# Kernel optimization log

Hardware: AMD Instinct MI355X
Metric: run time of the kernel (lower is better)

The kernel has to match this reference:

```python
import jax, jax.numpy as jnp
import numpy as np

B, T, D, H, L, V = 2, 1024, 768, 12, 8, 32000
HD = D // H


def setup_inputs() -> dict:
    key = jax.random.key(0)
    ks = jax.random.split(key, 16)
    init = lambda k, shape: jax.random.normal(k, shape, jnp.float32) * 0.02
    return {
        "idx": jax.random.randint(ks[0], (B, T), 0, V),
        "targets": jax.random.randint(ks[1], (B, T), 0, V),
        "tok_emb": init(ks[2], (V, D)),
        "pos_emb": init(ks[3], (T, D)),
        "ln1_w": jnp.ones((L, D)), "ln1_b": jnp.zeros((L, D)),
        "wq": init(ks[4], (L, D, D)),  # per-head D->HD projections stacked columnwise
        "wk": init(ks[5], (L, D, D)),
        "wv": init(ks[6], (L, D, D)),
        "wo": init(ks[7], (L, D, D)), "bo": jnp.zeros((L, D)),
        "ln2_w": jnp.ones((L, D)), "ln2_b": jnp.zeros((L, D)),
        "w1": init(ks[8], (L, D, 4 * D)), "b1": jnp.zeros((L, 4 * D)),
        "w2": init(ks[9], (L, 4 * D, D)), "b2": jnp.zeros((L, D)),
        "lnf_w": jnp.ones((D,)), "lnf_b": jnp.zeros((D,)),
        "lm_w": init(ks[10], (D, V)), "lm_b": jnp.zeros((V,)),
    }


def _ln(x, w, b):
    m = x.mean(-1, keepdims=True)
    v = x.var(-1, keepdims=True)
    return (x - m) * jax.lax.rsqrt(v + 1e-5) * w + b


def _gpt(idx, targets, tok_emb, pos_emb, ln1_w, ln1_b, wq, wk, wv, wo, bo,
         ln2_w, ln2_b, w1, b1, w2, b2, lnf_w, lnf_b, lm_w, lm_b):
    x = tok_emb[idx] + pos_emb[None, :T]          # [B,T,D]
    mask = jnp.tril(jnp.ones((T, T), bool))
    scale = D ** -0.5  # NOTE: original scales by embedding_dim**-0.5 (C), not head_size

    def block(x, p):
        l1w, l1b, Wq, Wk, Wv, Wo, Bo, l2w, l2b, W1, B1, W2, B2 = p
        h = _ln(x, l1w, l1b)
        q = (h @ Wq).reshape(B, T, H, HD)
        k = (h @ Wk).reshape(B, T, H, HD)
        v = (h @ Wv).reshape(B, T, H, HD)
        s = jnp.einsum('bqhd,bkhd->bhqk', q, k) * scale
        s = jnp.where(mask, s, -jnp.inf)
        a = jax.nn.softmax(s, axis=-1)
        o = jnp.einsum('bhqk,bkhd->bqhd', a, v).reshape(B, T, D)
        x = x + o @ Wo + Bo
        h = _ln(x, l2w, l2b)
        x = x + jax.nn.gelu(h @ W1 + B1, approximate=False) @ W2 + B2
        return x, None

    x, _ = jax.lax.scan(block, x, (ln1_w, ln1_b, wq, wk, wv, wo, bo,
                                   ln2_w, ln2_b, w1, b1, w2, b2))
    x = _ln(x, lnf_w, lnf_b)
    logits = (x @ lm_w + lm_b).reshape(B * T, V)
    logp = jax.nn.log_softmax(logits, axis=-1)
    loss = -jnp.take_along_axis(logp, targets.reshape(-1, 1), axis=1).mean()
    return logits, loss


def reference(idx, targets, tok_emb, pos_emb, ln1_w, ln1_b, wq, wk, wv, wo, bo,
              ln2_w, ln2_b, w1, b1, w2, b2, lnf_w, lnf_b, lm_w, lm_b):
    return _gpt(idx, targets, tok_emb, pos_emb, ln1_w, ln1_b, wq, wk, wv, wo, bo,
                ln2_w, ln2_b, w1, b1, w2, b2, lnf_w, lnf_b, lm_w, lm_b)
```

## Files before the change

kernel.cpp:

```cpp
#include <hip/hip_runtime.h>

#define Bz   2
#define Tz   1024
#define Dz   768
#define Hz   12
#define HDz  64
#define Lz   8
#define Vz   32000
#define BTz  (Bz*Tz)
#define DFz  (4*Dz)
#define SCALEz 0.036084391824351615f

typedef __attribute__((ext_vector_type(4))) short s16x4;
typedef __attribute__((ext_vector_type(8))) short s16x8;
typedef __attribute__((ext_vector_type(4))) float f32x4;

__device__ __forceinline__ short f2b(float f) {
    union { float f; unsigned u; } v; v.f = f;
    unsigned r = v.u + 0x7fffu + ((v.u >> 16) & 1u);
    return (short)(r >> 16);
}

__device__ __forceinline__ void gload16(const short* g, short* l) {
    __builtin_amdgcn_global_load_lds(
        (const __attribute__((address_space(1))) void*)g,
        (__attribute__((address_space(3))) void*)l, 16, 0, 0);
}

#define MFMA32(a,b,c) __builtin_amdgcn_mfma_f32_16x16x32_bf16(a,b,c,0,0,0)

__global__ __launch_bounds__(256)
void tconv_k(const float* __restrict__ in, short* __restrict__ out,
             int K, int N, int ldin)
{
    __shared__ float tl[32][33];
    const int tx = threadIdx.x & 31, ty = threadIdx.x >> 5;
    const int n0 = blockIdx.x * 32, k0 = blockIdx.y * 32;
    #pragma unroll
    for (int i = 0; i < 4; i++)
        tl[ty + i*8][tx] = in[(long)(k0 + ty + i*8)*ldin + n0 + tx];
    __syncthreads();
    #pragma unroll
    for (int i = 0; i < 4; i++)
        out[(long)(n0 + ty + i*8)*K + k0 + tx] = f2b(tl[tx][ty + i*8]);
}

template<int BM, int EPI, bool OUTBF>
__global__ __launch_bounds__(256)
void gemm2(const short* __restrict__ A, const short* __restrict__ Bt,
           const float* __restrict__ bias, const float* __restrict__ resp,
           void* __restrict__ Cv, int K, int ldc)
{
    constexpr int BN = 128, BK = 64;
    constexpr int WTM = BM/2;
    constexpr int AM = WTM/16;
    __shared__ short Al[BM*BK];
    __shared__ short Bl[BN*BK];
    const int m0 = blockIdx.y*BM, n0 = blockIdx.x*BN;
    const int tid = threadIdx.x, lane = tid & 63, wid = tid >> 6;
    const int wm = wid >> 1, wn = wid & 1;
    const int r = lane & 15, kg = lane >> 4;
    const int arow = lane >> 3, acol = (lane & 7)*8;

    const short* ga = A  + (long)(m0 + wid*(BM/4) + arow)*K + acol;
    const short* gb = Bt + (long)(n0 + wid*32     + arow)*K + acol;
    short* la = &Al[(wid*(BM/4))*BK];
    short* lb = &Bl[(wid*32)*BK];

    f32x4 acc[AM][4] = {};

    for (int k0 = 0; k0 < K; k0 += BK) {
        #pragma unroll
        for (int i = 0; i < BM/32; i++)
            gload16(ga + (long)i*8*K + k0, la + i*8*BK);
        #pragma unroll
        for (int i = 0; i < 4; i++)
            gload16(gb + (long)i*8*K + k0, lb + i*8*BK);
        __syncthreads();
        #pragma unroll
        for (int ks = 0; ks < 2; ks++) {
            s16x8 af[AM], bf[4];
            #pragma unroll
            for (int mI = 0; mI < AM; mI++)
                af[mI] = *(const s16x8*)&Al[(wm*WTM + mI*16 + r)*BK + ks*32 + kg*8];
            #pragma unroll
            for (int nI = 0; nI < 4; nI++)
                bf[nI] = *(const s16x8*)&Bl[(wn*64 + nI*16 + r)*BK + ks*32 + kg*8];
            #pragma unroll
            for (int mI = 0; mI < AM; mI++)
                #pragma unroll
                for (int nI = 0; nI < 4; nI++)
                    acc[mI][nI] = MFMA32(af[mI], bf[nI], acc[mI][nI]);
        }
        __syncthreads();
    }

    #pragma unroll
    for (int mI = 0; mI < AM; mI++) {
        #pragma unroll
        for (int nI = 0; nI < 4; nI++) {
            #pragma unroll
            for (int reg = 0; reg < 4; reg++) {
                int row = wm*WTM + mI*16 + kg*4 + reg;
                int col = wn*64 + nI*16 + r;
                long off = (long)(m0+row)*ldc + (n0+col);
                float v = acc[mI][nI][reg];
                if constexpr (EPI >= 1) v += bias[n0+col];
                if constexpr (EPI == 2) v += resp[off];
                if constexpr (EPI == 3) v = 0.5f*v*(1.0f + erff(v*0.70710678118654752f));
                if constexpr (OUTBF) ((short*)Cv)[off] = f2b(v);
                else                 ((float*)Cv)[off] = v;
            }
        }
    }
}

__global__ __launch_bounds__(256)
void attn_k(const short* __restrict__ qkv, short* __restrict__ att)
{
    const int w = threadIdx.x >> 6;
    const int lane = threadIdx.x & 63;
    const int r = lane & 15, kg = lane >> 4;
    const int hd0 = blockIdx.y * HDz;
    const long brow = (long)blockIdx.z * Tz;
    const int q0w = blockIdx.x * 64 + w * 16;
    const int qi = q0w + r;

    const short* qp = qkv + (brow + q0w + r) * 2304 + hd0;
    const s16x8 qf0 = *(const s16x8*)(qp + kg*8);
    const s16x8 qf1 = *(const s16x8*)(qp + 32 + kg*8);
    const short* kb = qkv + brow * 2304 + 768 + hd0;
    const short* vb = qkv + brow * 2304 + 1536 + hd0;

    float m = -3.4e38f, l = 0.f;
    f32x4 ot[4] = {};

    const int ntiles = blockIdx.x * 4 + w + 1;
    for (int t = 0; t < ntiles; t++) {
        const int kt = t * 16;
        const short* kp = kb + (long)(kt + r) * 2304;
        s16x8 kf0 = *(const s16x8*)(kp + kg*8);
        s16x8 kf1 = *(const s16x8*)(kp + 32 + kg*8);
        f32x4 z = {};
        f32x4 st = MFMA32(kf0, qf0, z);
        st = MFMA32(kf1, qf1, st);
        float s4[4];
        #pragma unroll
        for (int j = 0; j < 4; j++) {
            int ki = kt + kg*4 + j;
            s4[j] = (ki <= qi) ? st[j]*SCALEz : -1e30f;
        }
        float cm = fmaxf(fmaxf(s4[0], s4[1]), fmaxf(s4[2], s4[3]));
        cm = fmaxf(cm, __shfl_xor(cm, 16));
        cm = fmaxf(cm, __shfl_xor(cm, 32));
        float mn = fmaxf(m, cm);
        float alpha = __expf(m - mn);
        float p0 = __expf(s4[0]-mn), p1 = __expf(s4[1]-mn);
        float p2 = __expf(s4[2]-mn), p3 = __expf(s4[3]-mn);
        l = l*alpha + (p0+p1+p2+p3);
        m = mn;
        s16x8 pb = { f2b(p0), f2b(p1), f2b(p2), f2b(p3), 0, 0, 0, 0 };
        #pragma unroll
        for (int d0 = 0; d0 < 4; d0++) {
            const short* vp = vb + (long)(kt + kg*4)*2304 + d0*16 + r;
            s16x8 va = { vp[0], vp[2304], vp[4608], vp[6912], 0, 0, 0, 0 };
            f32x4 o = ot[d0];
            o[0]*=alpha; o[1]*=alpha; o[2]*=alpha; o[3]*=alpha;
            ot[d0] = MFMA32(va, pb, o);
        }
    }
    l += __shfl_xor(l, 16);
    l += __shfl_xor(l, 32);
    const float inv = 1.f / l;
    short* ap = att + (brow + q0w + r)*Dz + hd0;
    #pragma unroll
    for (int d0 = 0; d0 < 4; d0++)
        #pragma unroll
        for (int j = 0; j < 4; j++)
            ap[d0*16 + kg*4 + j] = f2b(ot[d0][j]*inv);
}

__global__ void embed_k(const int* __restrict__ idx, const float* __restrict__ tok,
                        const float* __restrict__ pos, float* __restrict__ x)
{
    int qi = blockIdx.x*blockDim.x + threadIdx.x;
    if (qi >= BTz*(Dz/4)) return;
    int row = qi / (Dz/4);
    int c   = (qi % (Dz/4)) * 4;
    int token = idx[row];
    int tpos  = row & (Tz-1);
    float4 a = *reinterpret_cast<const float4*>(tok + (long)token*Dz + c);
    float4 p = *reinterpret_cast<const float4*>(pos + (long)tpos*Dz + c);
    float4 o; o.x=a.x+p.x; o.y=a.y+p.y; o.z=a.z+p.z; o.w=a.w+p.w;
    *reinterpret_cast<float4*>(x + (long)row*Dz + c) = o;
}

__global__ __launch_bounds__(256)
void ln_k(const float* __restrict__ x, const float* __restrict__ w,
          const float* __restrict__ b, short* __restrict__ y)
{
    int row = blockIdx.x;
    const float* xr = x + (long)row*Dz;
    int t = threadIdx.x;
    float v0 = xr[t], v1 = xr[t+256], v2 = xr[t+512];
    __shared__ float s1[256], s2[256];
    s1[t] = v0+v1+v2;
    s2[t] = v0*v0+v1*v1+v2*v2;
    __syncthreads();
    for (int k = 128; k > 0; k >>= 1) {
        if (t < k) { s1[t] += s1[t+k]; s2[t] += s2[t+k]; }
        __syncthreads();
    }
    float mean = s1[0] * (1.0f/Dz);
    float var  = s2[0] * (1.0f/Dz) - mean*mean;
    float rs = rsqrtf(var + 1e-5f);
    short* yr = y + (long)row*Dz;
    yr[t]     = f2b((v0-mean)*rs*w[t]     + b[t]);
    yr[t+256] = f2b((v1-mean)*rs*w[t+256] + b[t+256]);
    yr[t+512] = f2b((v2-mean)*rs*w[t+512] + b[t+512]);
}

__global__ void loss_rows_k(const float* __restrict__ logits, const int* __restrict__ tgt,
                            float* __restrict__ row_loss)
{
    int row = blockIdx.x;
    const float* lr = logits + (long)row*Vz;
    int t = threadIdx.x;
    __shared__ float sm[256];
    float mx = -3.4e38f;
    for (int c = t; c < Vz; c += 256) mx = fmaxf(mx, lr[c]);
    sm[t] = mx; __syncthreads();
    for (int k = 128; k > 0; k >>= 1) { if (t < k) sm[t] = fmaxf(sm[t], sm[t+k]); __syncthreads(); }
    float m = sm[0]; __syncthreads();
    float s = 0.f;
    for (int c = t; c < Vz; c += 256) s += expf(lr[c]-m);
    sm[t] = s; __syncthreads();
    for (int k = 128; k > 0; k >>= 1) { if (t < k) sm[t] += sm[t+k]; __syncthreads(); }
    if (t == 0) {
        float logZ = m + logf(sm[0]);
        row_loss[row] = logZ - lr[tgt[row]];
    }
}

__global__ void loss_reduce_k(const float* __restrict__ row_loss, float* __restrict__ out)
{
    __shared__ float sm[256];
    int t = threadIdx.x;
    float s = 0.f;
    for (int i = t; i < BTz; i += 256) s += row_loss[i];
    sm[t] = s; __syncthreads();
    for (int k = 128; k > 0; k >>= 1) { if (t < k) sm[t] += sm[t+k]; __syncthreads(); }
    if (t == 0) out[0] = sm[0] * (1.0f/BTz);
}

extern "C" void kernel_launch(void* const* d_in, const int* in_sizes, int n_in,
                              void* d_out, int out_size, void* d_ws, size_t ws_size,
                              hipStream_t stream)
{
    const int*   idx     = (const int*)  d_in[0];
    const int*   tgt     = (const int*)  d_in[1];
    const float* tok_emb = (const float*)d_in[2];
    const float* pos_emb = (const float*)d_in[3];
    const float* ln1_w   = (const float*)d_in[4];
    const float* ln1_b   = (const float*)d_in[5];
    const float* wq      = (const float*)d_in[6];
    const float* wk      = (const float*)d_in[7];
    const float* wv      = (const float*)d_in[8];
    const float* wo      = (const float*)d_in[9];
    const float* bo      = (const float*)d_in[10];
    const float* ln2_w   = (const float*)d_in[11];
    const float* ln2_b   = (const float*)d_in[12];
    const float* w1      = (const float*)d_in[13];
    const float* b1      = (const float*)d_in[14];
    const float* w2      = (const float*)d_in[15];
    const float* b2      = (const float*)d_in[16];
    const float* lnf_w   = (const float*)d_in[17];
    const float* lnf_b   = (const float*)d_in[18];
    const float* lm_w    = (const float*)d_in[19];
    const float* lm_b    = (const float*)d_in[20];

    float* logits = (float*)d_out;
    float* loss   = logits + (long)BTz*Vz;

    float* x     = (float*)d_ws;
    float* rloss = x + (long)BTz*Dz;
    short* h     = (short*)(rloss + BTz);
    short* qkvb  = h    + (long)BTz*Dz;
    short* attb  = qkvb + (long)BTz*2304;
    short* midb  = attb + (long)BTz*Dz;
    short* wbuf  = midb + (long)BTz*DFz;
    short* qkvw  = wbuf;
    short* w1t   = wbuf + 2304*768;
    short* w2t   = w1t  + 3072*768;
    short* wot   = w2t  + 768*3072;

    embed_k<<<dim3((BTz*(Dz/4) + 255)/256), 256, 0, stream>>>(idx, tok_emb, pos_emb, x);

    for (int l = 0; l < Lz; l++) {
        const long wsz = (long)Dz*Dz;
        tconv_k<<<dim3(24,24), 256, 0, stream>>>(wq + l*wsz, qkvw,            Dz, Dz, Dz);
        tconv_k<<<dim3(24,24), 256, 0, stream>>>(wk + l*wsz, qkvw + 768*768,  Dz, Dz, Dz);
        tconv_k<<<dim3(24,24), 256, 0, stream>>>(wv + l*wsz, qkvw + 1536*768, Dz, Dz, Dz);
        tconv_k<<<dim3(24,24), 256, 0, stream>>>(wo + l*wsz, wot, Dz, Dz, Dz);
        tconv_k<<<dim3(96,24), 256, 0, stream>>>(w1 + (long)l*Dz*DFz, w1t, Dz, DFz, DFz);
        tconv_k<<<dim3(24,96), 256, 0, stream>>>(w2 + (long)l*Dz*DFz, w2t, DFz, Dz, Dz);

        ln_k<<<BTz, 256, 0, stream>>>(x, ln1_w + l*Dz, ln1_b + l*Dz, h);
        gemm2<128,0,true ><<<dim3(18,16), 256, 0, stream>>>(h, qkvw, nullptr, nullptr, qkvb, Dz, 2304);
        attn_k<<<dim3(Tz/64, Hz, Bz), 256, 0, stream>>>(qkvb, attb);
        gemm2<64, 2,false><<<dim3(6,32),  256, 0, stream>>>(attb, wot, bo + l*Dz, x, x, Dz, Dz);
        ln_k<<<BTz, 256, 0, stream>>>(x, ln2_w + l*Dz, ln2_b + l*Dz, h);
        gemm2<128,3,true ><<<dim3(24,16), 256, 0, stream>>>(h, w1t, b1 + l*DFz, nullptr, midb, Dz, DFz);
        gemm2<64, 2,false><<<dim3(6,32),  256, 0, stream>>>(midb, w2t, b2 + l*Dz, x, x, DFz, Dz);
    }

    ln_k<<<BTz, 256, 0, stream>>>(x, lnf_w, lnf_b, h);
    for (int c = 0; c < Vz; c += 8192) {
        int cn = (Vz - c < 8192) ? (Vz - c) : 8192;
        tconv_k<<<dim3(cn/32, 24), 256, 0, stream>>>(lm_w + c, wbuf, Dz, cn, Vz);
        gemm2<128,1,false><<<dim3(cn/128, 16), 256, 0, stream>>>(h, wbuf, lm_b + c, nullptr, logits + c, Dz, Vz);
    }

    loss_rows_k<<<BTz, 256, 0, stream>>>(logits, tgt, rloss);
    loss_reduce_k<<<1, 256, 0, stream>>>(rloss, loss);
}
```

Baseline: 1.878 ms.

## Batch weight conversion upfront, write transposed V from QKV GEMM, vectorize LN/loss

Weight transposition and bf16 conversion for all layers, plus the LM head, now run in one or two large launches up front when the workspace is big enough, replacing many small per-layer launches. The QKV GEMM epilogue writes V in a transposed layout, so attention loads V as contiguous 4-element vectors instead of strided scalars. LayerNorm maps one row per wavefront with float4 loads and shuffle reductions, and the loss and attention output paths use vectorized accesses. This costs extra workspace memory and keeps a fallback path for when the workspace is too small.

```diff
diff --git a/kernel.cpp b/kernel.cpp
--- a/kernel.cpp
+++ b/kernel.cpp
@@ -9,6 +9,7 @@
 #define Vz   32000
 #define BTz  (Bz*Tz)
 #define DFz  (4*Dz)
+#define PLWz 7077888L
 #define SCALEz 0.036084391824351615f
 
 typedef __attribute__((ext_vector_type(4))) short s16x4;
@@ -45,11 +46,45 @@
         out[(long)(n0 + ty + i*8)*K + k0 + tx] = f2b(tl[tx][ty + i*8]);
 }
 
-template<int BM, int EPI, bool OUTBF>
+__global__ __launch_bounds__(256)
+void wconv_all(const float* __restrict__ wq, const float* __restrict__ wk,
+               const float* __restrict__ wv, const float* __restrict__ wo,
+               const float* __restrict__ w1, const float* __restrict__ w2,
+               short* __restrict__ wall, int l0)
+{
+    const int l = l0 + blockIdx.y;
+    short* dst = wall + (long)blockIdx.y * PLWz;
+    int t = blockIdx.x;
+    const float* src; long doff; int K, N, ldin, nx;
+    if (t < 2304) {
+        int m = t / 576; t -= m * 576;
+        src = (m==0 ? wq : m==1 ? wk : m==2 ? wv : wo) + (long)l * 589824;
+        doff = (long)m * 589824; K = 768; N = 768; ldin = 768; nx = 24;
+    } else if (t < 4608) {
+        t -= 2304;
+        src = w1 + (long)l * 2359296; doff = 2359296; K = 768; N = 3072; ldin = 3072; nx = 96;
+    } else {
+        t -= 4608;
+        src = w2 + (long)l * 2359296; doff = 4718592; K = 3072; N = 768; ldin = 768; nx = 24;
+    }
+    const int n0 = (t % nx) * 32, k0 = (t / nx) * 32;
+    __shared__ float tl[32][33];
+    const int tx = threadIdx.x & 31, ty = threadIdx.x >> 5;
+    #pragma unroll
+    for (int i = 0; i < 4; i++)
+        tl[ty + i*8][tx] = src[(long)(k0 + ty + i*8)*ldin + n0 + tx];
+    __syncthreads();
+    short* o = dst + doff;
+    #pragma unroll
+    for (int i = 0; i < 4; i++)
+        o[(long)(n0 + ty + i*8)*K + k0 + tx] = f2b(tl[tx][ty + i*8]);
+}
+
+template<int BM, int EPI, bool OUTBF, bool VTEP = false>
 __global__ __launch_bounds__(256)
 void gemm2(const short* __restrict__ A, const short* __restrict__ Bt,
            const float* __restrict__ bias, const float* __restrict__ resp,
-           void* __restrict__ Cv, int K, int ldc)
+           void* __restrict__ Cv, int K, int ldc, short* __restrict__ vtp)
 {
     constexpr int BN = 128, BK = 64;
     constexpr int WTM = BM/2;
@@ -95,6 +130,25 @@
         __syncthreads();
     }
 
+    if constexpr (VTEP) {
+        if (n0 >= 1536) {
+            #pragma unroll
+            for (int mI = 0; mI < AM; mI++) {
+                #pragma unroll
+                for (int nI = 0; nI < 4; nI++) {
+                    int row0 = wm*WTM + mI*16 + kg*4;
+                    int col  = n0 - 1536 + wn*64 + nI*16 + r;
+                    int gr = m0 + row0;
+                    int b = gr >> 10, t0 = gr & 1023;
+                    s16x4 pk = { f2b(acc[mI][nI][0]), f2b(acc[mI][nI][1]),
+                                 f2b(acc[mI][nI][2]), f2b(acc[mI][nI][3]) };
+                    *(s16x4*)(vtp + ((long)b*Dz + col)*Tz + t0) = pk;
+                }
+            }
+            return;
+        }
+    }
+
     #pragma unroll
     for (int mI = 0; mI < AM; mI++) {
         #pragma unroll
@@ -116,7 +170,8 @@
 }
 
 __global__ __launch_bounds__(256)
-void attn_k(const short* __restrict__ qkv, short* __restrict__ att)
+void attn_k(const short* __restrict__ qkv, const short* __restrict__ vt,
+            short* __restrict__ att)
 {
     const int w = threadIdx.x >> 6;
     const int lane = threadIdx.x & 63;
@@ -130,7 +185,7 @@
     const s16x8 qf0 = *(const s16x8*)(qp + kg*8);
     const s16x8 qf1 = *(const s16x8*)(qp + 32 + kg*8);
     const short* kb = qkv + brow * 2304 + 768 + hd0;
-    const short* vb = qkv + brow * 2304 + 1536 + hd0;
+    const short* vtb = vt + ((long)blockIdx.z*Dz + hd0)*Tz;
 
     float m = -3.4e38f, l = 0.f;
     f32x4 ot[4] = {};
@@ -162,8 +217,8 @@
         s16x8 pb = { f2b(p0), f2b(p1), f2b(p2), f2b(p3), 0, 0, 0, 0 };
         #pragma unroll
         for (int d0 = 0; d0 < 4; d0++) {
-            const short* vp = vb + (long)(kt + kg*4)*2304 + d0*16 + r;
-            s16x8 va = { vp[0], vp[2304], vp[4608], vp[6912], 0, 0, 0, 0 };
+            const s16x4 v4 = *(const s16x4*)(vtb + (long)(d0*16 + r)*Tz + kt + kg*4);
+            s16x8 va = { v4[0], v4[1], v4[2], v4[3], 0, 0, 0, 0 };
             f32x4 o = ot[d0];
             o[0]*=alpha; o[1]*=alpha; o[2]*=alpha; o[3]*=alpha;
             ot[d0] = MFMA32(va, pb, o);
@@ -174,10 +229,11 @@
     const float inv = 1.f / l;
     short* ap = att + (brow + q0w + r)*Dz + hd0;
     #pragma unroll
-    for (int d0 = 0; d0 < 4; d0++)
-        #pragma unroll
-        for (int j = 0; j < 4; j++)
-            ap[d0*16 + kg*4 + j] = f2b(ot[d0][j]*inv);
+    for (int d0 = 0; d0 < 4; d0++) {
+        s16x4 pk = { f2b(ot[d0][0]*inv), f2b(ot[d0][1]*inv),
+                     f2b(ot[d0][2]*inv), f2b(ot[d0][3]*inv) };
+        *(s16x4*)(ap + d0*16 + kg*4) = pk;
+    }
 }
 
 __global__ void embed_k(const int* __restrict__ idx, const float* __restrict__ tok,
@@ -199,41 +255,60 @@
 void ln_k(const float* __restrict__ x, const float* __restrict__ w,
           const float* __restrict__ b, short* __restrict__ y)
 {
-    int row = blockIdx.x;
+    const int lane = threadIdx.x & 63;
+    const int row = blockIdx.x*4 + (threadIdx.x >> 6);
     const float* xr = x + (long)row*Dz;
-    int t = threadIdx.x;
-    float v0 = xr[t], v1 = xr[t+256], v2 = xr[t+512];
-    __shared__ float s1[256], s2[256];
-    s1[t] = v0+v1+v2;
-    s2[t] = v0*v0+v1*v1+v2*v2;
-    __syncthreads();
-    for (int k = 128; k > 0; k >>= 1) {
-        if (t < k) { s1[t] += s1[t+k]; s2[t] += s2[t+k]; }
-        __syncthreads();
-    }
-    float mean = s1[0] * (1.0f/Dz);
-    float var  = s2[0] * (1.0f/Dz) - mean*mean;
+    float4 v[3];
+    #pragma unroll
+    for (int j = 0; j < 3; j++) v[j] = *(const float4*)(xr + lane*4 + j*256);
+    float s = 0.f, ss = 0.f;
+    #pragma unroll
+    for (int j = 0; j < 3; j++) {
+        s  += v[j].x + v[j].y + v[j].z + v[j].w;
+        ss += v[j].x*v[j].x + v[j].y*v[j].y + v[j].z*v[j].z + v[j].w*v[j].w;
+    }
+    #pragma unroll
+    for (int o = 32; o > 0; o >>= 1) {
+        s += __shfl_xor(s, o); ss += __shfl_xor(ss, o);
+    }
+    float mean = s * (1.0f/Dz);
+    float var  = ss * (1.0f/Dz) - mean*mean;
     float rs = rsqrtf(var + 1e-5f);
     short* yr = y + (long)row*Dz;
-    yr[t]     = f2b((v0-mean)*rs*w[t]     + b[t]);
-    yr[t+256] = f2b((v1-mean)*rs*w[t+256] + b[t+256]);
-    yr[t+512] = f2b((v2-mean)*rs*w[t+512] + b[t+512]);
-}
-
-__global__ void loss_rows_k(const float* __restrict__ logits, const int* __restrict__ tgt,
-                            float* __restrict__ row_loss)
+    #pragma unroll
+    for (int j = 0; j < 3; j++) {
+        float4 wj = *(const float4*)(w + lane*4 + j*256);
+        float4 bj = *(const float4*)(b + lane*4 + j*256);
+        s16x4 pk = { f2b((v[j].x-mean)*rs*wj.x + bj.x),
+                     f2b((v[j].y-mean)*rs*wj.y + bj.y),
+                     f2b((v[j].z-mean)*rs*wj.z + bj.z),
+                     f2b((v[j].w-mean)*rs*wj.w + bj.w) };
+        *(s16x4*)(yr + lane*4 + j*256) = pk;
+    }
+}
+
+__global__ __launch_bounds__(256)
+void loss_rows_k(const float* __restrict__ logits, const int* __restrict__ tgt,
+                 float* __restrict__ row_loss)
 {
     int row = blockIdx.x;
     const float* lr = logits + (long)row*Vz;
+    const float4* lr4 = (const float4*)lr;
     int t = threadIdx.x;
     __shared__ float sm[256];
     float mx = -3.4e38f;
-    for (int c = t; c < Vz; c += 256) mx = fmaxf(mx, lr[c]);
+    for (int c = t; c < Vz/4; c += 256) {
+        float4 f = lr4[c];
+        mx = fmaxf(mx, fmaxf(fmaxf(f.x, f.y), fmaxf(f.z, f.w)));
+    }
     sm[t] = mx; __syncthreads();
     for (int k = 128; k > 0; k >>= 1) { if (t < k) sm[t] = fmaxf(sm[t], sm[t+k]); __syncthreads(); }
     float m = sm[0]; __syncthreads();
     float s = 0.f;
-    for (int c = t; c < Vz; c += 256) s += expf(lr[c]-m);
+    for (int c = t; c < Vz/4; c += 256) {
+        float4 f = lr4[c];
+        s += expf(f.x-m) + expf(f.y-m) + expf(f.z-m) + expf(f.w-m);
+    }
     sm[t] = s; __syncthreads();
     for (int k = 128; k > 0; k >>= 1) { if (t < k) sm[t] += sm[t+k]; __syncthreads(); }
     if (t == 0) {
@@ -282,43 +357,56 @@
     float* logits = (float*)d_out;
     float* loss   = logits + (long)BTz*Vz;
 
-    float* x     = (float*)d_ws;
-    float* rloss = x + (long)BTz*Dz;
-    short* h     = (short*)(rloss + BTz);
-    short* qkvb  = h    + (long)BTz*Dz;
-    short* attb  = qkvb + (long)BTz*2304;
-    short* midb  = attb + (long)BTz*Dz;
-    short* wbuf  = midb + (long)BTz*DFz;
-    short* qkvw  = wbuf;
-    short* w1t   = wbuf + 2304*768;
-    short* w2t   = w1t  + 3072*768;
-    short* wot   = w2t  + 768*3072;
+    char* p = (char*)d_ws;
+    float* x     = (float*)p; p += (long)BTz*Dz*4;
+    float* rloss = (float*)p; p += BTz*4;
+    short* h     = (short*)p; p += (long)BTz*Dz*2;
+    short* qkvb  = (short*)p; p += (long)BTz*2304*2;
+    short* vt    = (short*)p; p += (long)Bz*Dz*Tz*2;
+    short* attb  = (short*)p; p += (long)BTz*Dz*2;
+    short* midb  = (short*)p; p += (long)BTz*DFz*2;
+    short* wall  = (short*)p;
+    size_t fixed = (size_t)(p - (char*)d_ws);
+    const long LMT = (long)Vz*Dz;
+    bool upfront = ws_size >= fixed + (size_t)(8*PLWz + LMT)*2;
+    short* lmt = wall + (upfront ? 8*PLWz : PLWz);
 
     embed_k<<<dim3((BTz*(Dz/4) + 255)/256), 256, 0, stream>>>(idx, tok_emb, pos_emb, x);
 
+    if (upfront) {
+        wconv_all<<<dim3(6912, 8), 256, 0, stream>>>(wq, wk, wv, wo, w1, w2, wall, 0);
+        tconv_k<<<dim3(Vz/32, 24), 256, 0, stream>>>(lm_w, lmt, Dz, Vz, Vz);
+    }
+
     for (int l = 0; l < Lz; l++) {
-        const long wsz = (long)Dz*Dz;
-        tconv_k<<<dim3(24,24), 256, 0, stream>>>(wq + l*wsz, qkvw,            Dz, Dz, Dz);
-        tconv_k<<<dim3(24,24), 256, 0, stream>>>(wk + l*wsz, qkvw + 768*768,  Dz, Dz, Dz);
-        tconv_k<<<dim3(24,24), 256, 0, stream>>>(wv + l*wsz, qkvw + 1536*768, Dz, Dz, Dz);
-        tconv_k<<<dim3(24,24), 256, 0, stream>>>(wo + l*wsz, wot, Dz, Dz, Dz);
-        tconv_k<<<dim3(96,24), 256, 0, stream>>>(w1 + (long)l*Dz*DFz, w1t, Dz, DFz, DFz);
-        tconv_k<<<dim3(24,96), 256, 0, stream>>>(w2 + (long)l*Dz*DFz, w2t, DFz, Dz, Dz);
-
-        ln_k<<<BTz, 256, 0, stream>>>(x, ln1_w + l*Dz, ln1_b + l*Dz, h);
-        gemm2<128,0,true ><<<dim3(18,16), 256, 0, stream>>>(h, qkvw, nullptr, nullptr, qkvb, Dz, 2304);
-        attn_k<<<dim3(Tz/64, Hz, Bz), 256, 0, stream>>>(qkvb, attb);
-        gemm2<64, 2,false><<<dim3(6,32),  256, 0, stream>>>(attb, wot, bo + l*Dz, x, x, Dz, Dz);
-        ln_k<<<BTz, 256, 0, stream>>>(x, ln2_w + l*Dz, ln2_b + l*Dz, h);
-        gemm2<128,3,true ><<<dim3(24,16), 256, 0, stream>>>(h, w1t, b1 + l*DFz, nullptr, midb, Dz, DFz);
-        gemm2<64, 2,false><<<dim3(6,32),  256, 0, stream>>>(midb, w2t, b2 + l*Dz, x, x, DFz, Dz);
-    }
-
-    ln_k<<<BTz, 256, 0, stream>>>(x, lnf_w, lnf_b, h);
-    for (int c = 0; c < Vz; c += 8192) {
-        int cn = (Vz - c < 8192) ? (Vz - c) : 8192;
-        tconv_k<<<dim3(cn/32, 24), 256, 0, stream>>>(lm_w + c, wbuf, Dz, cn, Vz);
-        gemm2<128,1,false><<<dim3(cn/128, 16), 256, 0, stream>>>(h, wbuf, lm_b + c, nullptr, logits + c, Dz, Vz);
+        short* wl = wall + (upfront ? (long)l*PLWz : 0);
+        if (!upfront)
+            wconv_all<<<dim3(6912, 1), 256, 0, stream>>>(wq, wk, wv, wo, w1, w2, wall, l);
+
+        ln_k<<<BTz/4, 256, 0, stream>>>(x, ln1_w + l*Dz, ln1_b + l*Dz, h);
+        gemm2<128,0,true,true><<<dim3(18,16), 256, 0, stream>>>(
+            h, wl, nullptr, nullptr, qkvb, Dz, 2304, vt);
+        attn_k<<<dim3(Tz/64, Hz, Bz), 256, 0, stream>>>(qkvb, vt, attb);
+        gemm2<64,2,false><<<dim3(6,32), 256, 0, stream>>>(
+            attb, wl + 1769472, bo + l*Dz, x, x, Dz, Dz, nullptr);
+        ln_k<<<BTz/4, 256, 0, stream>>>(x, ln2_w + l*Dz, ln2_b + l*Dz, h);
+        gemm2<128,3,true><<<dim3(24,16), 256, 0, stream>>>(
+            h, wl + 2359296, b1 + l*DFz, nullptr, midb, Dz, DFz, nullptr);
+        gemm2<64,2,false><<<dim3(6,32), 256, 0, stream>>>(
+            midb, wl + 4718592, b2 + l*Dz, x, x, DFz, Dz, nullptr);
+    }
+
+    ln_k<<<BTz/4, 256, 0, stream>>>(x, lnf_w, lnf_b, h);
+    if (upfront) {
+        gemm2<128,1,false><<<dim3(Vz/128, 16), 256, 0, stream>>>(
+            h, lmt, lm_b, nullptr, logits, Dz, Vz, nullptr);
+    } else {
+        for (int c = 0; c < Vz; c += 8192) {
+            int cn = (Vz - c < 8192) ? (Vz - c) : 8192;
+            tconv_k<<<dim3(cn/32, 24), 256, 0, stream>>>(lm_w + c, lmt, Dz, cn, Vz);
+            gemm2<128,1,false><<<dim3(cn/128, 16), 256, 0, stream>>>(
+                h, lmt, lm_b + c, nullptr, logits + c, Dz, Vz, nullptr);
+        }
     }
 
     loss_rows_k<<<BTz, 256, 0, stream>>>(logits, tgt, rloss);
```

New measurement: 2.145 ms. +14.2%, slower.
